# Optimization experiments

Measured on AMD Instinct MI355X. Metric: run time of the kernel, lower is better.

## Reference

```python
import jax, jax.numpy as jnp
import numpy as np

D_MODEL = 1024
N_HEADS = 16
N_KV = 1          # MQA: the torch module only repeats xk_attn/sv, so n_kv must be 1 or n_heads
HEAD_DIM = 64     # d_model // total_n_heads
B = 1
L = 2048
SCALE = 1.0 / np.sqrt(HEAD_DIM)


def _rope(x, cos, sin):
    # x: [B, L, H, hd]; cos/sin: [L, hd//2]; pairs are consecutive elements (llama2.c style)
    xr, xi = x[..., 0::2], x[..., 1::2]
    c = cos[None, :, None, :]
    s = sin[None, :, None, :]
    out_r = xr * c - xi * s
    out_i = xr * s + xi * c
    return jnp.stack([out_r, out_i], axis=-1).reshape(x.shape)


def setup_inputs() -> dict:
    key = jax.random.key(0)
    ks = jax.random.split(key, 8)
    x = jax.random.normal(ks[0], (B, L, D_MODEL), dtype=jnp.float32)
    symbols = jax.random.normal(ks[1], (B, L, D_MODEL), dtype=jnp.float32)
    # standard RoPE frequencies
    inv_freq = 1.0 / (10000.0 ** (np.arange(0, HEAD_DIM, 2, dtype=np.float64) / HEAD_DIM))
    angles = np.outer(np.arange(L, dtype=np.float64), inv_freq)
    freqs_cos = jnp.asarray(np.cos(angles), dtype=jnp.float32)
    freqs_sin = jnp.asarray(np.sin(angles), dtype=jnp.float32)
    s = 0.02
    wq_attn = jax.random.normal(ks[2], (D_MODEL, N_HEADS * HEAD_DIM), dtype=jnp.float32) * s
    wk_attn = jax.random.normal(ks[3], (D_MODEL, N_KV * HEAD_DIM), dtype=jnp.float32) * s
    wq_rel = jax.random.normal(ks[4], (D_MODEL, N_HEADS * HEAD_DIM), dtype=jnp.float32) * s
    wk_rel = jax.random.normal(ks[5], (D_MODEL, N_KV * HEAD_DIM), dtype=jnp.float32) * s
    wv = jax.random.normal(ks[6], (D_MODEL, N_KV * HEAD_DIM), dtype=jnp.float32) * s
    wo = jax.random.normal(ks[7], (N_HEADS * HEAD_DIM, N_HEADS * HEAD_DIM), dtype=jnp.float32) * s
    return {"x": x, "symbols": symbols, "freqs_cos": freqs_cos, "freqs_sin": freqs_sin,
            "wq_attn": wq_attn, "wk_attn": wk_attn, "wq_rel": wq_rel, "wk_rel": wk_rel,
            "wv": wv, "wo": wo}


def reference(x, symbols, freqs_cos, freqs_sin, wq_attn, wk_attn, wq_rel, wk_rel, wv, wo):
    bsz, seqlen, _ = x.shape
    n_rep = N_HEADS // N_KV
    # projections
    xq_a = (x @ wq_attn).reshape(bsz, seqlen, N_HEADS, HEAD_DIM)
    xk_a = (x @ wk_attn).reshape(bsz, seqlen, N_KV, HEAD_DIM)
    xq_r = (x @ wq_rel).reshape(bsz, seqlen, N_HEADS, HEAD_DIM)
    xk_r = (x @ wk_rel).reshape(bsz, seqlen, N_KV, HEAD_DIM)
    sv = (symbols @ wv).reshape(bsz, seqlen, N_KV, HEAD_DIM)
    # RoPE only on attention q/k (matches torch code)
    xq_a = _rope(xq_a, freqs_cos, freqs_sin)
    xk_a = _rope(xk_a, freqs_cos, freqs_sin)
    # GQA/MQA head repetition of attn keys and symbol-values (NOT rel keys, per source)
    xk_a = jnp.repeat(xk_a, n_rep, axis=2)   # [B, L, H, hd]
    sv = jnp.repeat(sv, n_rep, axis=2)       # [B, L, H, hd]
    # attention scores with causal mask
    attn_scores = jnp.einsum('bihd,bjhd->bhij', xq_a, xk_a) * SCALE
    causal_bias = jnp.where(jnp.tril(jnp.ones((seqlen, seqlen), dtype=bool)),
                            jnp.float32(0.0), -jnp.inf)
    attn_scores = jax.nn.softmax(attn_scores + causal_bias, axis=-1)
    # relation scores: xk_r has N_KV=1 heads, broadcast against H query heads (identity activation)
    rel_scores = jnp.einsum('bihd,bjd->bhij', xq_r, xk_r[:, :, 0, :]) * SCALE
    rca_scores = attn_scores * rel_scores
    out = jnp.einsum('bhij,bjhd->bihd', rca_scores, sv)
    out = out.reshape(bsz, seqlen, N_HEADS * HEAD_DIM) @ wo
    return (out, attn_scores, rel_scores)
```

## Files before the change

kernel.cpp:

```cpp
#include <hip/hip_runtime.h>
#include <hip/hip_bf16.h>
#include <stdint.h>

#define LQ 2048
#define DM 1024
#define NH 16
#define HD 64
#define NPAIR 32
#define SCALE_F 0.125f

#define QROWS 16
__global__ __launch_bounds__(256) void k_proj_q(
    const float* __restrict__ x, const float* __restrict__ wqa, const float* __restrict__ wqr,
    const float* __restrict__ fcos, const float* __restrict__ fsin,
    float* __restrict__ Qa, float* __restrict__ Qr)
{
    __shared__ float xS[QROWS * DM];
    const int bid = blockIdx.x;
    const int i0 = (bid >> 2) * QROWS;
    const int m = (bid >> 1) & 1;
    const int half = bid & 1;
    const int tid = threadIdx.x;
    {
        const float4* src = (const float4*)(x + (size_t)i0 * DM);
        float4* dst4 = (float4*)xS;
        for (int t = tid; t < QROWS * DM / 4; t += 256) dst4[t] = src[t];
    }
    __syncthreads();
    const int q = half * 256 + tid;
    const float2* __restrict__ w2 = (const float2*)(m ? wqr : wqa);
    float ae[QROWS], ao[QROWS];
#pragma unroll
    for (int r = 0; r < QROWS; ++r) { ae[r] = 0.f; ao[r] = 0.f; }
    for (int k = 0; k < DM; k += 4) {
        float2 w0 = w2[(size_t)(k + 0) * (DM / 2) + q];
        float2 w1 = w2[(size_t)(k + 1) * (DM / 2) + q];
        float2 w2v = w2[(size_t)(k + 2) * (DM / 2) + q];
        float2 w3 = w2[(size_t)(k + 3) * (DM / 2) + q];
#pragma unroll
        for (int r = 0; r < QROWS; ++r) {
            float4 xv = *(const float4*)&xS[r * DM + k];
            ae[r] = fmaf(xv.x, w0.x, ae[r]);  ao[r] = fmaf(xv.x, w0.y, ao[r]);
            ae[r] = fmaf(xv.y, w1.x, ae[r]);  ao[r] = fmaf(xv.y, w1.y, ao[r]);
            ae[r] = fmaf(xv.z, w2v.x, ae[r]); ao[r] = fmaf(xv.z, w2v.y, ao[r]);
            ae[r] = fmaf(xv.w, w3.x, ae[r]);  ao[r] = fmaf(xv.w, w3.y, ao[r]);
        }
    }
    float* __restrict__ dst = m ? Qr : Qa;
    const int p = q & (NPAIR - 1);
#pragma unroll
    for (int r = 0; r < QROWS; ++r) {
        float oe = ae[r], oo = ao[r];
        if (m == 0) {
            float c = fcos[(i0 + r) * NPAIR + p];
            float s = fsin[(i0 + r) * NPAIR + p];
            oe = ae[r] * c - ao[r] * s;
            oo = ae[r] * s + ao[r] * c;
        }
        *(float2*)&dst[(size_t)(i0 + r) * DM + 2 * q] = make_float2(oe, oo);
    }
}

#define KVROWS 8
__global__ __launch_bounds__(128) void k_proj_kv(
    const float* __restrict__ x, const float* __restrict__ symbols,
    const float* __restrict__ wka, const float* __restrict__ wkr, const float* __restrict__ wv,
    const float* __restrict__ fcos, const float* __restrict__ fsin,
    float* __restrict__ Ka, float* __restrict__ Kr, float* __restrict__ SV)
{
    __shared__ float xS[KVROWS * DM], sS[KVROWS * DM];
    const int i0 = blockIdx.x * KVROWS;
    const int tid = threadIdx.x;
    {
        const float4* sx = (const float4*)(x + (size_t)i0 * DM);
        const float4* ss = (const float4*)(symbols + (size_t)i0 * DM);
        for (int t = tid; t < KVROWS * DM / 4; t += 128) {
            ((float4*)xS)[t] = sx[t];
            ((float4*)sS)[t] = ss[t];
        }
    }
    __syncthreads();
    if (tid >= 96) return;
    const int m = tid >> 5;
    const int p = tid & 31;
    const float2* __restrict__ w2 = (const float2*)(m == 0 ? wka : (m == 1 ? wkr : wv));
    const float* __restrict__ src = (m == 2) ? sS : xS;
    float ae[KVROWS], ao[KVROWS];
#pragma unroll
    for (int r = 0; r < KVROWS; ++r) { ae[r] = 0.f; ao[r] = 0.f; }
    for (int k = 0; k < DM; ++k) {
        float2 w = w2[k * 32 + p];
#pragma unroll
        for (int r = 0; r < KVROWS; ++r) {
            float xv = src[r * DM + k];
            ae[r] = fmaf(xv, w.x, ae[r]);
            ao[r] = fmaf(xv, w.y, ao[r]);
        }
    }
    float* __restrict__ dst = (m == 0 ? Ka : (m == 1 ? Kr : SV));
#pragma unroll
    for (int r = 0; r < KVROWS; ++r) {
        float oe = ae[r], oo = ao[r];
        if (m == 0) {
            float c = fcos[(i0 + r) * NPAIR + p];
            float s = fsin[(i0 + r) * NPAIR + p];
            oe = ae[r] * c - ao[r] * s;
            oo = ae[r] * s + ao[r] * c;
        }
        dst[(i0 + r) * HD + 2 * p] = oe;
        dst[(i0 + r) * HD + 2 * p + 1] = oo;
    }
}

__global__ __launch_bounds__(256) void k_rel(
    const float* __restrict__ Qr, const float* __restrict__ Kr, float* __restrict__ relout)
{
    __shared__ float QS[64][65];
    __shared__ float KS[64][65];
    const int j0 = blockIdx.x * 64, i0 = blockIdx.y * 64, h = blockIdx.z;
    const int tid = threadIdx.x;
    for (int t = tid; t < 64 * 64; t += 256) {
        int r = t >> 6, c = t & 63;
        QS[r][c] = Qr[(size_t)(i0 + r) * DM + h * HD + c];
        KS[r][c] = Kr[(j0 + r) * HD + c];
    }
    __syncthreads();
    const int ti = tid & 15, tj = tid >> 4;
    float acc[4][4] = {};
    for (int d = 0; d < HD; ++d) {
        float qv[4], kv[4];
#pragma unroll
        for (int a = 0; a < 4; ++a) qv[a] = QS[ti * 4 + a][d];
#pragma unroll
        for (int b = 0; b < 4; ++b) kv[b] = KS[tj * 4 + b][d];
#pragma unroll
        for (int a = 0; a < 4; ++a)
#pragma unroll
            for (int b = 0; b < 4; ++b) acc[a][b] = fmaf(qv[a], kv[b], acc[a][b]);
    }
#pragma unroll
    for (int a = 0; a < 4; ++a) {
        float4 w = make_float4(acc[a][0] * SCALE_F, acc[a][1] * SCALE_F,
                               acc[a][2] * SCALE_F, acc[a][3] * SCALE_F);
        *(float4*)&relout[(size_t)(h * LQ + i0 + ti * 4 + a) * LQ + j0 + tj * 4] = w;
    }
}

__global__ __launch_bounds__(256) void k_attn_fused(
    const float* __restrict__ Qa, const float* __restrict__ Ka, const float* __restrict__ SV,
    const float* __restrict__ relin, float* __restrict__ attnout,
    float* __restrict__ Lrow, float* __restrict__ OutH)
{
    __shared__ float QS[64 * 65];
    __shared__ float KSbuf[64 * 68];
    __shared__ float SVS[64 * 68];
    const int bid = blockIdx.x;
    const int h = bid & 15;
    const int it = 31 - (bid >> 4);
    const int i0 = it * 64;
    const int tid = threadIdx.x;
    for (int t = tid; t < 64 * 64; t += 256) {
        int r = t >> 6, c = t & 63;
        QS[r * 65 + c] = Qa[(size_t)(i0 + r) * DM + h * HD + c];
    }
    const int ti = tid & 15, tj = tid >> 4;
    float l_[4] = {0.f, 0.f, 0.f, 0.f};
    float oacc[4][4] = {};
    for (int jt = 0; jt <= it; ++jt) {
        const int j0 = jt * 64;
        __syncthreads();
        for (int t = tid; t < 64 * 16; t += 256) {
            int r = t >> 4, c4 = (t & 15) << 2;
            *(float4*)&KSbuf[r * 68 + c4] = *(const float4*)&Ka[(j0 + r) * HD + c4];
            *(float4*)&SVS[r * 68 + c4]  = *(const float4*)&SV[(j0 + r) * HD + c4];
        }
        const int jb = j0 + tj * 4;
        float4 rv[4];
#pragma unroll
        for (int a = 0; a < 4; ++a)
            rv[a] = *(const float4*)&relin[(size_t)(h * LQ + i0 + ti * 4 + a) * LQ + jb];
        __syncthreads();
        float s[4][4] = {};
        for (int d = 0; d < HD; ++d) {
            float qv[4], kv[4];
#pragma unroll
            for (int a = 0; a < 4; ++a) qv[a] = QS[(ti * 4 + a) * 65 + d];
#pragma unroll
            for (int b = 0; b < 4; ++b) kv[b] = KSbuf[(tj * 4 + b) * 68 + d];
#pragma unroll
            for (int a = 0; a < 4; ++a)
#pragma unroll
                for (int b = 0; b < 4; ++b) s[a][b] = fmaf(qv[a], kv[b], s[a][b]);
        }
        __syncthreads();
        float* pS = KSbuf;
#pragma unroll
        for (int a = 0; a < 4; ++a) {
            const int i = i0 + ti * 4 + a;
            const float* rl = (const float*)&rv[a];
            float e[4];
#pragma unroll
            for (int b = 0; b < 4; ++b) {
                int j = jb + b;
                e[b] = (j <= i) ? __expf(s[a][b] * SCALE_F) : 0.f;
                l_[a] += e[b];
                pS[(ti * 4 + a) * 65 + tj * 4 + b] = e[b] * rl[b];
            }
            *(float4*)&attnout[(size_t)(h * LQ + i) * LQ + jb] =
                make_float4(e[0], e[1], e[2], e[3]);
        }
        __syncthreads();
        for (int j = 0; j < 64; ++j) {
            float4 sv4 = *(const float4*)&SVS[j * 68 + tj * 4];
            float pv[4];
#pragma unroll
            for (int a = 0; a < 4; ++a) pv[a] = pS[(ti * 4 + a) * 65 + j];
#pragma unroll
            for (int a = 0; a < 4; ++a) {
                oacc[a][0] = fmaf(pv[a], sv4.x, oacc[a][0]);
                oacc[a][1] = fmaf(pv[a], sv4.y, oacc[a][1]);
                oacc[a][2] = fmaf(pv[a], sv4.z, oacc[a][2]);
                oacc[a][3] = fmaf(pv[a], sv4.w, oacc[a][3]);
            }
        }
    }
    __syncthreads();
    float* red = SVS;
#pragma unroll
    for (int a = 0; a < 4; ++a) red[(ti * 4 + a) * 17 + tj] = l_[a];
    __syncthreads();
    if (tid < 64) {
        float Ls = 0.f;
        for (int t = 0; t < 16; ++t) Ls += red[tid * 17 + t];
        red[tid * 17 + 16] = Ls;
        Lrow[h * LQ + i0 + tid] = Ls;
    }
    __syncthreads();
#pragma unroll
    for (int a = 0; a < 4; ++a) {
        float inv = 1.0f / red[(ti * 4 + a) * 17 + 16];
        float4 v = make_float4(oacc[a][0] * inv, oacc[a][1] * inv,
                               oacc[a][2] * inv, oacc[a][3] * inv);
        *(float4*)&OutH[(size_t)(i0 + ti * 4 + a) * DM + h * HD + tj * 4] = v;
    }
}

__global__ __launch_bounds__(256) void k_attn_norm(
    const float* __restrict__ Lrow, float* __restrict__ attnout)
{
    const int i = blockIdx.x & (LQ - 1);
    const int h = blockIdx.x >> 11;
    const float inv = 1.0f / Lrow[h * LQ + i];
    float* __restrict__ row = attnout + (size_t)(h * LQ + i) * LQ;
    const int tid = threadIdx.x;
    for (int c4 = tid; c4 < LQ / 4; c4 += 256) {
        const int c = c4 * 4;
        if (c + 3 <= i) {
            float4 v = *(const float4*)&row[c];
            v.x *= inv; v.y *= inv; v.z *= inv; v.w *= inv;
            *(float4*)&row[c] = v;
        } else if (c > i) {
            *(float4*)&row[c] = make_float4(0.f, 0.f, 0.f, 0.f);
        } else {
            float4 v = *(const float4*)&row[c];
            float4 o;
            o.x = (c + 0 <= i) ? v.x * inv : 0.f;
            o.y = (c + 1 <= i) ? v.y * inv : 0.f;
            o.z = (c + 2 <= i) ? v.z * inv : 0.f;
            o.w = (c + 3 <= i) ? v.w * inv : 0.f;
            *(float4*)&row[c] = o;
        }
    }
}

__global__ __launch_bounds__(256) void k_outproj(
    const float* __restrict__ OutH, const float* __restrict__ wo, float* __restrict__ outp)
{
    __shared__ float AS[64][65];
    __shared__ float BS[64][65];
    const int n0 = blockIdx.x * 64, i0 = blockIdx.y * 64;
    const int tid = threadIdx.x;
    const int ti = tid & 15, tj = tid >> 4;
    float acc[4][4] = {};
    for (int kt = 0; kt < DM / 64; ++kt) {
        const int k0 = kt * 64;
        __syncthreads();
        for (int t = tid; t < 64 * 64; t += 256) {
            int r = t >> 6, c = t & 63;
            AS[r][c] = OutH[(size_t)(i0 + r) * DM + k0 + c];
            BS[r][c] = wo[(size_t)(k0 + r) * DM + n0 + c];
        }
        __syncthreads();
        for (int kk = 0; kk < 64; ++kk) {
            float av[4], bv[4];
#pragma unroll
            for (int a = 0; a < 4; ++a) av[a] = AS[ti * 4 + a][kk];
#pragma unroll
            for (int b = 0; b < 4; ++b) bv[b] = BS[kk][tj * 4 + b];
#pragma unroll
            for (int a = 0; a < 4; ++a)
#pragma unroll
                for (int b = 0; b < 4; ++b) acc[a][b] = fmaf(av[a], bv[b], acc[a][b]);
        }
    }
#pragma unroll
    for (int a = 0; a < 4; ++a) {
        float4 v = make_float4(acc[a][0], acc[a][1], acc[a][2], acc[a][3]);
        *(float4*)&outp[(size_t)(i0 + ti * 4 + a) * DM + n0 + tj * 4] = v;
    }
}

extern "C" void kernel_launch(void* const* d_in, const int* in_sizes, int n_in,
                              void* d_out, int out_size, void* d_ws, size_t ws_size,
                              hipStream_t stream)
{
    const float* x       = (const float*)d_in[0];
    const float* symbols = (const float*)d_in[1];
    const float* fcos    = (const float*)d_in[2];
    const float* fsin    = (const float*)d_in[3];
    const float* wqa     = (const float*)d_in[4];
    const float* wka     = (const float*)d_in[5];
    const float* wqr     = (const float*)d_in[6];
    const float* wkr     = (const float*)d_in[7];
    const float* wv      = (const float*)d_in[8];
    const float* wo      = (const float*)d_in[9];

    float* out_main = (float*)d_out;
    float* out_attn = out_main + (size_t)LQ * DM;
    float* out_rel  = out_attn + (size_t)NH * LQ * LQ;

    float* ws   = (float*)d_ws;
    float* Qa   = ws;
    float* Qr   = Qa + (size_t)LQ * DM;
    float* Ka   = Qr + (size_t)LQ * DM;
    float* Kr   = Ka + (size_t)LQ * HD;
    float* SV   = Kr + (size_t)LQ * HD;
    float* Mrow = SV + (size_t)LQ * HD;
    float* Lrow = Mrow + (size_t)NH * LQ;
    float* OutH = Lrow + (size_t)NH * LQ;

    k_proj_q<<<dim3((LQ / QROWS) * 4), 256, 0, stream>>>(x, wqa, wqr, fcos, fsin, Qa, Qr);
    k_proj_kv<<<dim3(LQ / KVROWS), 128, 0, stream>>>(x, symbols, wka, wkr, wv, fcos, fsin, Ka, Kr, SV);
    k_rel<<<dim3(32, 32, 16), 256, 0, stream>>>(Qr, Kr, out_rel);
    k_attn_fused<<<dim3(32 * 16), 256, 0, stream>>>(Qa, Ka, SV, out_rel, out_attn, Lrow, OutH);
    k_attn_norm<<<dim3(NH * LQ), 256, 0, stream>>>(Lrow, out_attn);
    k_outproj<<<dim3(16, 32), 256, 0, stream>>>(OutH, wo, out_main);
}
```

Baseline: 1.363 ms.

## Fuse attn normalization into attention kernel and vectorize LDS inner loops

Removes the separate k_attn_norm launch. The attention kernel now rescales its own attention rows after computing row sums and zero-fills the masked upper region. The rel, attention and outproj kernels move to float4 LDS reads with a 68-float stride and a strided row mapping (ti+16*a). k_rel now computes 128-row tiles, and attention blocks are reordered to mix light and heavy causal tiles. The in-kernel normalization re-reads each row from global memory while the same block still runs, and lengthens the tail of the blocks with the most work.

```diff
diff --git a/kernel.cpp b/kernel.cpp
--- a/kernel.cpp
+++ b/kernel.cpp
@@ -115,57 +115,67 @@
 __global__ __launch_bounds__(256) void k_rel(
     const float* __restrict__ Qr, const float* __restrict__ Kr, float* __restrict__ relout)
 {
-    __shared__ float QS[64][65];
-    __shared__ float KS[64][65];
-    const int j0 = blockIdx.x * 64, i0 = blockIdx.y * 64, h = blockIdx.z;
-    const int tid = threadIdx.x;
-    for (int t = tid; t < 64 * 64; t += 256) {
-        int r = t >> 6, c = t & 63;
-        QS[r][c] = Qr[(size_t)(i0 + r) * DM + h * HD + c];
-        KS[r][c] = Kr[(j0 + r) * HD + c];
+    __shared__ float QS[128 * 68];
+    __shared__ float KS[64 * 68];
+    const int j0 = blockIdx.x * 64, i0 = blockIdx.y * 128, h = blockIdx.z;
+    const int tid = threadIdx.x;
+    for (int t = tid; t < 128 * 16; t += 256) {
+        int r = t >> 4, c4 = (t & 15) << 2;
+        *(float4*)&QS[r * 68 + c4] = *(const float4*)&Qr[(size_t)(i0 + r) * DM + h * HD + c4];
+    }
+    for (int t = tid; t < 64 * 16; t += 256) {
+        int r = t >> 4, c4 = (t & 15) << 2;
+        *(float4*)&KS[r * 68 + c4] = *(const float4*)&Kr[(j0 + r) * HD + c4];
     }
     __syncthreads();
     const int ti = tid & 15, tj = tid >> 4;
-    float acc[4][4] = {};
-    for (int d = 0; d < HD; ++d) {
-        float qv[4], kv[4];
-#pragma unroll
-        for (int a = 0; a < 4; ++a) qv[a] = QS[ti * 4 + a][d];
-#pragma unroll
-        for (int b = 0; b < 4; ++b) kv[b] = KS[tj * 4 + b][d];
-#pragma unroll
-        for (int a = 0; a < 4; ++a)
-#pragma unroll
-            for (int b = 0; b < 4; ++b) acc[a][b] = fmaf(qv[a], kv[b], acc[a][b]);
-    }
-#pragma unroll
-    for (int a = 0; a < 4; ++a) {
+    float acc[8][4] = {};
+#pragma unroll 2
+    for (int d = 0; d < HD; d += 4) {
+        float4 kv[4];
+#pragma unroll
+        for (int b = 0; b < 4; ++b) kv[b] = *(const float4*)&KS[(tj * 4 + b) * 68 + d];
+#pragma unroll
+        for (int a = 0; a < 8; ++a) {
+            float4 qv = *(const float4*)&QS[(ti + 16 * a) * 68 + d];
+#pragma unroll
+            for (int b = 0; b < 4; ++b) {
+                acc[a][b] = fmaf(qv.x, kv[b].x, acc[a][b]);
+                acc[a][b] = fmaf(qv.y, kv[b].y, acc[a][b]);
+                acc[a][b] = fmaf(qv.z, kv[b].z, acc[a][b]);
+                acc[a][b] = fmaf(qv.w, kv[b].w, acc[a][b]);
+            }
+        }
+    }
+#pragma unroll
+    for (int a = 0; a < 8; ++a) {
         float4 w = make_float4(acc[a][0] * SCALE_F, acc[a][1] * SCALE_F,
                                acc[a][2] * SCALE_F, acc[a][3] * SCALE_F);
-        *(float4*)&relout[(size_t)(h * LQ + i0 + ti * 4 + a) * LQ + j0 + tj * 4] = w;
+        *(float4*)&relout[(size_t)(h * LQ + i0 + ti + 16 * a) * LQ + j0 + tj * 4] = w;
     }
 }
 
 __global__ __launch_bounds__(256) void k_attn_fused(
     const float* __restrict__ Qa, const float* __restrict__ Ka, const float* __restrict__ SV,
-    const float* __restrict__ relin, float* __restrict__ attnout,
-    float* __restrict__ Lrow, float* __restrict__ OutH)
-{
-    __shared__ float QS[64 * 65];
+    const float* __restrict__ relin, float* __restrict__ attnout, float* __restrict__ OutH)
+{
+    __shared__ float QS[64 * 68];
     __shared__ float KSbuf[64 * 68];
     __shared__ float SVS[64 * 68];
     const int bid = blockIdx.x;
     const int h = bid & 15;
-    const int it = 31 - (bid >> 4);
+    const int m = bid >> 4;
+    const int it = (m < 16) ? m : 47 - m;
     const int i0 = it * 64;
     const int tid = threadIdx.x;
-    for (int t = tid; t < 64 * 64; t += 256) {
-        int r = t >> 6, c = t & 63;
-        QS[r * 65 + c] = Qa[(size_t)(i0 + r) * DM + h * HD + c];
+    for (int t = tid; t < 64 * 16; t += 256) {
+        int r = t >> 4, c4 = (t & 15) << 2;
+        *(float4*)&QS[r * 68 + c4] = *(const float4*)&Qa[(size_t)(i0 + r) * DM + h * HD + c4];
     }
     const int ti = tid & 15, tj = tid >> 4;
     float l_[4] = {0.f, 0.f, 0.f, 0.f};
     float oacc[4][4] = {};
+    float* pS = KSbuf;
     for (int jt = 0; jt <= it; ++jt) {
         const int j0 = jt * 64;
         __syncthreads();
@@ -178,97 +188,100 @@
         float4 rv[4];
 #pragma unroll
         for (int a = 0; a < 4; ++a)
-            rv[a] = *(const float4*)&relin[(size_t)(h * LQ + i0 + ti * 4 + a) * LQ + jb];
+            rv[a] = *(const float4*)&relin[(size_t)(h * LQ + i0 + ti + 16 * a) * LQ + jb];
         __syncthreads();
         float s[4][4] = {};
-        for (int d = 0; d < HD; ++d) {
-            float qv[4], kv[4];
-#pragma unroll
-            for (int a = 0; a < 4; ++a) qv[a] = QS[(ti * 4 + a) * 65 + d];
-#pragma unroll
-            for (int b = 0; b < 4; ++b) kv[b] = KSbuf[(tj * 4 + b) * 68 + d];
-#pragma unroll
-            for (int a = 0; a < 4; ++a)
-#pragma unroll
-                for (int b = 0; b < 4; ++b) s[a][b] = fmaf(qv[a], kv[b], s[a][b]);
-        }
-        __syncthreads();
-        float* pS = KSbuf;
+#pragma unroll 2
+        for (int d = 0; d < HD; d += 4) {
+            float4 kv[4];
+#pragma unroll
+            for (int b = 0; b < 4; ++b) kv[b] = *(const float4*)&KSbuf[(tj * 4 + b) * 68 + d];
+#pragma unroll
+            for (int a = 0; a < 4; ++a) {
+                float4 qv = *(const float4*)&QS[(ti + 16 * a) * 68 + d];
+#pragma unroll
+                for (int b = 0; b < 4; ++b) {
+                    s[a][b] = fmaf(qv.x, kv[b].x, s[a][b]);
+                    s[a][b] = fmaf(qv.y, kv[b].y, s[a][b]);
+                    s[a][b] = fmaf(qv.z, kv[b].z, s[a][b]);
+                    s[a][b] = fmaf(qv.w, kv[b].w, s[a][b]);
+                }
+            }
+        }
+        __syncthreads();
 #pragma unroll
         for (int a = 0; a < 4; ++a) {
-            const int i = i0 + ti * 4 + a;
+            const int i = i0 + ti + 16 * a;
             const float* rl = (const float*)&rv[a];
-            float e[4];
-#pragma unroll
-            for (int b = 0; b < 4; ++b) {
-                int j = jb + b;
-                e[b] = (j <= i) ? __expf(s[a][b] * SCALE_F) : 0.f;
-                l_[a] += e[b];
-                pS[(ti * 4 + a) * 65 + tj * 4 + b] = e[b] * rl[b];
+            float e0 = (jb + 0 <= i) ? __expf(s[a][0] * SCALE_F) : 0.f;
+            float e1 = (jb + 1 <= i) ? __expf(s[a][1] * SCALE_F) : 0.f;
+            float e2 = (jb + 2 <= i) ? __expf(s[a][2] * SCALE_F) : 0.f;
+            float e3 = (jb + 3 <= i) ? __expf(s[a][3] * SCALE_F) : 0.f;
+            l_[a] += e0 + e1 + e2 + e3;
+            *(float4*)&pS[(ti + 16 * a) * 68 + tj * 4] =
+                make_float4(e0 * rl[0], e1 * rl[1], e2 * rl[2], e3 * rl[3]);
+            *(float4*)&attnout[(size_t)(h * LQ + i) * LQ + jb] =
+                make_float4(e0, e1, e2, e3);
+        }
+        __syncthreads();
+#pragma unroll 2
+        for (int g = 0; g < 64; g += 4) {
+            float4 sv0 = *(const float4*)&SVS[(g + 0) * 68 + tj * 4];
+            float4 sv1 = *(const float4*)&SVS[(g + 1) * 68 + tj * 4];
+            float4 sv2 = *(const float4*)&SVS[(g + 2) * 68 + tj * 4];
+            float4 sv3 = *(const float4*)&SVS[(g + 3) * 68 + tj * 4];
+#pragma unroll
+            for (int a = 0; a < 4; ++a) {
+                float4 p4 = *(const float4*)&pS[(ti + 16 * a) * 68 + g];
+                oacc[a][0] = fmaf(p4.x, sv0.x, oacc[a][0]);
+                oacc[a][1] = fmaf(p4.x, sv0.y, oacc[a][1]);
+                oacc[a][2] = fmaf(p4.x, sv0.z, oacc[a][2]);
+                oacc[a][3] = fmaf(p4.x, sv0.w, oacc[a][3]);
+                oacc[a][0] = fmaf(p4.y, sv1.x, oacc[a][0]);
+                oacc[a][1] = fmaf(p4.y, sv1.y, oacc[a][1]);
+                oacc[a][2] = fmaf(p4.y, sv1.z, oacc[a][2]);
+                oacc[a][3] = fmaf(p4.y, sv1.w, oacc[a][3]);
+                oacc[a][0] = fmaf(p4.z, sv2.x, oacc[a][0]);
+                oacc[a][1] = fmaf(p4.z, sv2.y, oacc[a][1]);
+                oacc[a][2] = fmaf(p4.z, sv2.z, oacc[a][2]);
+                oacc[a][3] = fmaf(p4.z, sv2.w, oacc[a][3]);
+                oacc[a][0] = fmaf(p4.w, sv3.x, oacc[a][0]);
+                oacc[a][1] = fmaf(p4.w, sv3.y, oacc[a][1]);
+                oacc[a][2] = fmaf(p4.w, sv3.z, oacc[a][2]);
+                oacc[a][3] = fmaf(p4.w, sv3.w, oacc[a][3]);
             }
-            *(float4*)&attnout[(size_t)(h * LQ + i) * LQ + jb] =
-                make_float4(e[0], e[1], e[2], e[3]);
-        }
-        __syncthreads();
-        for (int j = 0; j < 64; ++j) {
-            float4 sv4 = *(const float4*)&SVS[j * 68 + tj * 4];
-            float pv[4];
-#pragma unroll
-            for (int a = 0; a < 4; ++a) pv[a] = pS[(ti * 4 + a) * 65 + j];
-#pragma unroll
-            for (int a = 0; a < 4; ++a) {
-                oacc[a][0] = fmaf(pv[a], sv4.x, oacc[a][0]);
-                oacc[a][1] = fmaf(pv[a], sv4.y, oacc[a][1]);
-                oacc[a][2] = fmaf(pv[a], sv4.z, oacc[a][2]);
-                oacc[a][3] = fmaf(pv[a], sv4.w, oacc[a][3]);
-            }
         }
     }
     __syncthreads();
     float* red = SVS;
 #pragma unroll
-    for (int a = 0; a < 4; ++a) red[(ti * 4 + a) * 17 + tj] = l_[a];
+    for (int a = 0; a < 4; ++a) red[(ti + 16 * a) * 17 + tj] = l_[a];
     __syncthreads();
     if (tid < 64) {
         float Ls = 0.f;
+#pragma unroll
         for (int t = 0; t < 16; ++t) Ls += red[tid * 17 + t];
-        red[tid * 17 + 16] = Ls;
-        Lrow[h * LQ + i0 + tid] = Ls;
+        red[tid * 17 + 16] = 1.0f / Ls;
     }
     __syncthreads();
 #pragma unroll
     for (int a = 0; a < 4; ++a) {
-        float inv = 1.0f / red[(ti * 4 + a) * 17 + 16];
-        float4 v = make_float4(oacc[a][0] * inv, oacc[a][1] * inv,
-                               oacc[a][2] * inv, oacc[a][3] * inv);
-        *(float4*)&OutH[(size_t)(i0 + ti * 4 + a) * DM + h * HD + tj * 4] = v;
-    }
-}
-
-__global__ __launch_bounds__(256) void k_attn_norm(
-    const float* __restrict__ Lrow, float* __restrict__ attnout)
-{
-    const int i = blockIdx.x & (LQ - 1);
-    const int h = blockIdx.x >> 11;
-    const float inv = 1.0f / Lrow[h * LQ + i];
-    float* __restrict__ row = attnout + (size_t)(h * LQ + i) * LQ;
-    const int tid = threadIdx.x;
-    for (int c4 = tid; c4 < LQ / 4; c4 += 256) {
-        const int c = c4 * 4;
-        if (c + 3 <= i) {
-            float4 v = *(const float4*)&row[c];
+        float inv = red[(ti + 16 * a) * 17 + 16];
+        *(float4*)&OutH[(size_t)(i0 + ti + 16 * a) * DM + h * HD + tj * 4] =
+            make_float4(oacc[a][0] * inv, oacc[a][1] * inv,
+                        oacc[a][2] * inv, oacc[a][3] * inv);
+    }
+    const int lastc4 = (it + 1) * 16;
+    for (int idx = tid; idx < 64 * (LQ / 4); idx += 256) {
+        const int r = idx >> 9, c4 = idx & 511;
+        float* p = &attnout[(size_t)(h * LQ + i0 + r) * LQ + (c4 << 2)];
+        if (c4 < lastc4) {
+            const float inv = red[r * 17 + 16];
+            float4 v = *(const float4*)p;
             v.x *= inv; v.y *= inv; v.z *= inv; v.w *= inv;
-            *(float4*)&row[c] = v;
-        } else if (c > i) {
-            *(float4*)&row[c] = make_float4(0.f, 0.f, 0.f, 0.f);
+            *(float4*)p = v;
         } else {
-            float4 v = *(const float4*)&row[c];
-            float4 o;
-            o.x = (c + 0 <= i) ? v.x * inv : 0.f;
-            o.y = (c + 1 <= i) ? v.y * inv : 0.f;
-            o.z = (c + 2 <= i) ? v.z * inv : 0.f;
-            o.w = (c + 3 <= i) ? v.w * inv : 0.f;
-            *(float4*)&row[c] = o;
+            *(float4*)p = make_float4(0.f, 0.f, 0.f, 0.f);
         }
     }
 }
@@ -276,8 +289,8 @@
 __global__ __launch_bounds__(256) void k_outproj(
     const float* __restrict__ OutH, const float* __restrict__ wo, float* __restrict__ outp)
 {
-    __shared__ float AS[64][65];
-    __shared__ float BS[64][65];
+    __shared__ float AS[64 * 68];
+    __shared__ float BS[64 * 68];
     const int n0 = blockIdx.x * 64, i0 = blockIdx.y * 64;
     const int tid = threadIdx.x;
     const int ti = tid & 15, tj = tid >> 4;
@@ -285,28 +298,36 @@
     for (int kt = 0; kt < DM / 64; ++kt) {
         const int k0 = kt * 64;
         __syncthreads();
-        for (int t = tid; t < 64 * 64; t += 256) {
-            int r = t >> 6, c = t & 63;
-            AS[r][c] = OutH[(size_t)(i0 + r) * DM + k0 + c];
-            BS[r][c] = wo[(size_t)(k0 + r) * DM + n0 + c];
-        }
-        __syncthreads();
-        for (int kk = 0; kk < 64; ++kk) {
-            float av[4], bv[4];
-#pragma unroll
-            for (int a = 0; a < 4; ++a) av[a] = AS[ti * 4 + a][kk];
-#pragma unroll
-            for (int b = 0; b < 4; ++b) bv[b] = BS[kk][tj * 4 + b];
-#pragma unroll
-            for (int a = 0; a < 4; ++a)
-#pragma unroll
-                for (int b = 0; b < 4; ++b) acc[a][b] = fmaf(av[a], bv[b], acc[a][b]);
+        for (int t = tid; t < 64 * 16; t += 256) {
+            int r = t >> 4, c4 = (t & 15) << 2;
+            *(float4*)&AS[r * 68 + c4] = *(const float4*)&OutH[(size_t)(i0 + r) * DM + k0 + c4];
+            *(float4*)&BS[r * 68 + c4] = *(const float4*)&wo[(size_t)(k0 + r) * DM + n0 + c4];
+        }
+        __syncthreads();
+#pragma unroll 2
+        for (int kk = 0; kk < 64; kk += 4) {
+            float4 b0 = *(const float4*)&BS[(kk + 0) * 68 + tj * 4];
+            float4 b1 = *(const float4*)&BS[(kk + 1) * 68 + tj * 4];
+            float4 b2 = *(const float4*)&BS[(kk + 2) * 68 + tj * 4];
+            float4 b3 = *(const float4*)&BS[(kk + 3) * 68 + tj * 4];
+#pragma unroll
+            for (int a = 0; a < 4; ++a) {
+                float4 av = *(const float4*)&AS[(ti + 16 * a) * 68 + kk];
+                acc[a][0] = fmaf(av.x, b0.x, acc[a][0]); acc[a][1] = fmaf(av.x, b0.y, acc[a][1]);
+                acc[a][2] = fmaf(av.x, b0.z, acc[a][2]); acc[a][3] = fmaf(av.x, b0.w, acc[a][3]);
+                acc[a][0] = fmaf(av.y, b1.x, acc[a][0]); acc[a][1] = fmaf(av.y, b1.y, acc[a][1]);
+                acc[a][2] = fmaf(av.y, b1.z, acc[a][2]); acc[a][3] = fmaf(av.y, b1.w, acc[a][3]);
+                acc[a][0] = fmaf(av.z, b2.x, acc[a][0]); acc[a][1] = fmaf(av.z, b2.y, acc[a][1]);
+                acc[a][2] = fmaf(av.z, b2.z, acc[a][2]); acc[a][3] = fmaf(av.z, b2.w, acc[a][3]);
+                acc[a][0] = fmaf(av.w, b3.x, acc[a][0]); acc[a][1] = fmaf(av.w, b3.y, acc[a][1]);
+                acc[a][2] = fmaf(av.w, b3.z, acc[a][2]); acc[a][3] = fmaf(av.w, b3.w, acc[a][3]);
+            }
         }
     }
 #pragma unroll
     for (int a = 0; a < 4; ++a) {
-        float4 v = make_float4(acc[a][0], acc[a][1], acc[a][2], acc[a][3]);
-        *(float4*)&outp[(size_t)(i0 + ti * 4 + a) * DM + n0 + tj * 4] = v;
+        *(float4*)&outp[(size_t)(i0 + ti + 16 * a) * DM + n0 + tj * 4] =
+            make_float4(acc[a][0], acc[a][1], acc[a][2], acc[a][3]);
     }
 }
 
@@ -341,8 +362,7 @@
 
     k_proj_q<<<dim3((LQ / QROWS) * 4), 256, 0, stream>>>(x, wqa, wqr, fcos, fsin, Qa, Qr);
     k_proj_kv<<<dim3(LQ / KVROWS), 128, 0, stream>>>(x, symbols, wka, wkr, wv, fcos, fsin, Ka, Kr, SV);
-    k_rel<<<dim3(32, 32, 16), 256, 0, stream>>>(Qr, Kr, out_rel);
-    k_attn_fused<<<dim3(32 * 16), 256, 0, stream>>>(Qa, Ka, SV, out_rel, out_attn, Lrow, OutH);
-    k_attn_norm<<<dim3(NH * LQ), 256, 0, stream>>>(Lrow, out_attn);
+    k_rel<<<dim3(32, 16, 16), 256, 0, stream>>>(Qr, Kr, out_rel);
+    k_attn_fused<<<dim3(32 * 16), 256, 0, stream>>>(Qa, Ka, SV, out_rel, out_attn, OutH);
     k_outproj<<<dim3(16, 32), 256, 0, stream>>>(OutH, wo, out_main);
 }
```

Result: faster. 1.263 ms (-7.4%).
